# Kernel tuning notes

Measured on AMD Instinct MI355X. Metric: run time of the kernel, lower is better.

Reference implementation:

```python
import jax, jax.numpy as jnp
import numpy as np

B, C, H, W = 4, 4, 1080, 1920


def setup_inputs() -> dict:
    key = jax.random.key(0)
    k1, k2 = jax.random.split(key)
    frame = jax.random.normal(k1, (B, C, H, W), dtype=jnp.float32)
    flow = jax.random.normal(k2, (B, 2, H, W), dtype=jnp.float32)
    return {"frame": frame, "flow": flow}


def _bilinear_warp(frame, flow):
    # TF-addons style dense_image_warp: sample frame at (y - flow_y, x - flow_x),
    # query points clamped to the image rectangle, bilinear interpolation.
    b, c, h, w = frame.shape
    gy = jnp.arange(h, dtype=flow.dtype)
    gx = jnp.arange(w, dtype=flow.dtype)
    qy = jnp.clip(gy[None, :, None] - flow[:, 0], 0.0, h - 1)  # [B,H,W]
    qx = jnp.clip(gx[None, None, :] - flow[:, 1], 0.0, w - 1)  # [B,H,W]
    y0f = jnp.floor(qy)
    x0f = jnp.floor(qx)
    wy = (qy - y0f)[:, None]  # [B,1,H,W]
    wx = (qx - x0f)[:, None]
    y0 = y0f.astype(jnp.int32)
    x0 = x0f.astype(jnp.int32)
    y1 = jnp.minimum(y0 + 1, h - 1)
    x1 = jnp.minimum(x0 + 1, w - 1)
    ff = frame.reshape(b, c, h * w)

    def gather(y, x):
        idx = (y * w + x).reshape(b, 1, h * w)
        return jnp.take_along_axis(ff, idx, axis=2).reshape(b, c, h, w)

    top = gather(y0, x0) * (1.0 - wx) + gather(y0, x1) * wx
    bot = gather(y1, x0) * (1.0 - wx) + gather(y1, x1) * wx
    return top * (1.0 - wy) + bot * wy


def reference(frame, flow):
    return _bilinear_warp(frame, flow)
```

## Files before the change

kernel.cpp:

```cpp
#include <hip/hip_runtime.h>


#define BB 4
#define CC 4
#define HH 1080
#define WW 1920
#define HW (HH * WW)
#define NPIX (BB * HH * WW)
#define NBLK (NPIX / 256)

typedef float f32x2 __attribute__((ext_vector_type(2), aligned(4)));

__global__ __launch_bounds__(256) void dense_warp_kernel(
    const float* __restrict__ frame,
    const float* __restrict__ flow,
    float* __restrict__ out)
{
    const int n   = blockIdx.x;
    const int blk = (n & 7) * (NBLK >> 3) + (n >> 3);

    const int p = blk * 256 + threadIdx.x;
    const int x = p % WW;
    const int t = p / WW;
    const int y = t % HH;
    const int b = t / HH;

    const size_t rowoff = (size_t)y * WW + x;
    const float fy = flow[(size_t)(b * 2 + 0) * HW + rowoff];
    const float fx = flow[(size_t)(b * 2 + 1) * HW + rowoff];

    const float qy = fminf(fmaxf((float)y - fy, 0.0f), (float)(HH - 1));
    const float qx = fminf(fmaxf((float)x - fx, 0.0f), (float)(WW - 1));
    const float y0f = floorf(qy);
    const float x0f = floorf(qx);
    const float wy = qy - y0f;
    float       wx = qx - x0f;
    const int y0 = (int)y0f;
    const int x0 = (int)x0f;
    const int y1 = min(y0 + 1, HH - 1);

    const bool edge = (x0 > WW - 2);
    const int  xb   = edge ? (WW - 2) : x0;
    if (edge) wx = 1.0f;

    const int i0 = y0 * WW + xb;
    const int i1 = y1 * WW + xb;

    const float omwx = 1.0f - wx;
    const float omwy = 1.0f - wy;

#pragma unroll
    for (int c = 0; c < CC; ++c) {
        const float* fp = frame + (size_t)(b * CC + c) * HW;
        const f32x2 t2 = *reinterpret_cast<const f32x2*>(fp + i0);
        const f32x2 b2 = *reinterpret_cast<const f32x2*>(fp + i1);
        const float top = t2.x * omwx + t2.y * wx;
        const float bot = b2.x * omwx + b2.y * wx;
        const float v   = top * omwy + bot * wy;
        __builtin_nontemporal_store(v, out + (size_t)(b * CC + c) * HW + rowoff);
    }
}

extern "C" void kernel_launch(void* const* d_in, const int* in_sizes, int n_in,
                              void* d_out, int out_size, void* d_ws, size_t ws_size,
                              hipStream_t stream)
{
    const float* frame = (const float*)d_in[0];
    const float* flow  = (const float*)d_in[1];
    float* out = (float*)d_out;

    dense_warp_kernel<<<NBLK, 256, 0, stream>>>(frame, flow, out);
}
```

Baseline: 76.65 us.

## Stage frame tiles with halo in LDS for bilinear gathers

Each block now handles a 128x12 output tile and first loads a haloed 23x140 patch of all four channels into shared memory. Bilinear samples whose footprint falls inside the staged patch are read from LDS, and the rest fall back to global memory. The aim is to turn scattered global gathers into cheap LDS reads, since standard-normal flow mostly displaces by only a few pixels. In exchange it adds a staging pass that reads roughly double the tile area, a block-wide barrier, lower occupancy from about 51 KB of LDS per block, and branch divergence on the fallback path.

After: 161.0 us. 110% more time.

```diff
diff --git a/kernel.cpp b/kernel.cpp
--- a/kernel.cpp
+++ b/kernel.cpp
@@ -6,58 +6,118 @@
 #define HH 1080
 #define WW 1920
 #define HW (HH * WW)
-#define NPIX (BB * HH * WW)
-#define NBLK (NPIX / 256)
 
-typedef float f32x2 __attribute__((ext_vector_type(2), aligned(4)));
+#define TW 128
+#define TH 12
+#define MARG 5
+#define RST 23
+#define CST 140
+#define CUSE 139
+#define TILES_X (WW / TW)
+#define TILES_Y (HH / TH)
+#define NBLK (BB * TILES_Y * TILES_X)
+#define STAGE_N (CC * RST * CST)
 
 __global__ __launch_bounds__(256) void dense_warp_kernel(
     const float* __restrict__ frame,
     const float* __restrict__ flow,
     float* __restrict__ out)
 {
+    __shared__ float lds[STAGE_N];
+
     const int n   = blockIdx.x;
     const int blk = (n & 7) * (NBLK >> 3) + (n >> 3);
 
-    const int p = blk * 256 + threadIdx.x;
-    const int x = p % WW;
-    const int t = p / WW;
-    const int y = t % HH;
-    const int b = t / HH;
+    const int txi = blk % TILES_X;
+    const int t2  = blk / TILES_X;
+    const int tyi = t2 % TILES_Y;
+    const int b   = t2 / TILES_Y;
 
-    const size_t rowoff = (size_t)y * WW + x;
-    const float fy = flow[(size_t)(b * 2 + 0) * HW + rowoff];
-    const float fx = flow[(size_t)(b * 2 + 1) * HW + rowoff];
+    const int tx = txi * TW;
+    const int ty = tyi * TH;
+    const int row_base = ty - MARG;
+    const int col_base = tx - MARG;
 
-    const float qy = fminf(fmaxf((float)y - fy, 0.0f), (float)(HH - 1));
-    const float qx = fminf(fmaxf((float)x - fx, 0.0f), (float)(WW - 1));
-    const float y0f = floorf(qy);
-    const float x0f = floorf(qx);
-    const float wy = qy - y0f;
-    float       wx = qx - x0f;
-    const int y0 = (int)y0f;
-    const int x0 = (int)x0f;
-    const int y1 = min(y0 + 1, HH - 1);
+    const float* fb = frame + (size_t)b * CC * HW;
 
-    const bool edge = (x0 > WW - 2);
-    const int  xb   = edge ? (WW - 2) : x0;
-    if (edge) wx = 1.0f;
+    for (int idx = threadIdx.x; idx < STAGE_N; idx += 256) {
+        const int col = idx % CST;
+        const int tt  = idx / CST;
+        const int r   = tt % RST;
+        const int c   = tt / RST;
+        const int grow = min(max(row_base + r, 0), HH - 1);
+        const int gcol = min(max(col_base + col, 0), WW - 1);
+        lds[idx] = fb[(size_t)c * HW + grow * WW + gcol];
+    }
+    __syncthreads();
 
-    const int i0 = y0 * WW + xb;
-    const int i1 = y1 * WW + xb;
-
-    const float omwx = 1.0f - wx;
-    const float omwy = 1.0f - wy;
+    const int x_local = threadIdx.x & (TW - 1);
+    const int rg      = threadIdx.x >> 7;
+    const int x       = tx + x_local;
 
 #pragma unroll
-    for (int c = 0; c < CC; ++c) {
-        const float* fp = frame + (size_t)(b * CC + c) * HW;
-        const f32x2 t2 = *reinterpret_cast<const f32x2*>(fp + i0);
-        const f32x2 b2 = *reinterpret_cast<const f32x2*>(fp + i1);
-        const float top = t2.x * omwx + t2.y * wx;
-        const float bot = b2.x * omwx + b2.y * wx;
-        const float v   = top * omwy + bot * wy;
-        __builtin_nontemporal_store(v, out + (size_t)(b * CC + c) * HW + rowoff);
+    for (int r = 0; r < TH / 2; ++r) {
+        const int y = ty + rg * (TH / 2) + r;
+        const size_t rowoff = (size_t)y * WW + x;
+
+        const float fy = flow[(size_t)(b * 2 + 0) * HW + rowoff];
+        const float fx = flow[(size_t)(b * 2 + 1) * HW + rowoff];
+
+        const float qy  = fminf(fmaxf((float)y - fy, 0.0f), (float)(HH - 1));
+        const float qx  = fminf(fmaxf((float)x - fx, 0.0f), (float)(WW - 1));
+        const float y0f = floorf(qy);
+        const float x0f = floorf(qx);
+        const float wy  = qy - y0f;
+        float       wx  = qx - x0f;
+        const int y0 = (int)y0f;
+        const int x0 = (int)x0f;
+        const int y1 = min(y0 + 1, HH - 1);
+
+        const bool edge = (x0 > WW - 2);
+        const int  xb   = edge ? (WW - 2) : x0;
+        if (edge) wx = 1.0f;
+
+        const float omwx = 1.0f - wx;
+        const float omwy = 1.0f - wy;
+
+        const int sy0 = y0 - row_base;
+        const int sy1 = y1 - row_base;
+        const int sx  = xb - col_base;
+
+        float res[CC];
+        if (sy0 >= 0 && sy1 < RST && sx >= 0 && sx < CUSE - 1) {
+            const int itop = sy0 * CST + sx;
+            const int ibot = sy1 * CST + sx;
+#pragma unroll
+            for (int c = 0; c < CC; ++c) {
+                const float* p  = lds + c * (RST * CST);
+                const float t0 = p[itop];
+                const float t1 = p[itop + 1];
+                const float b0 = p[ibot];
+                const float b1 = p[ibot + 1];
+                res[c] = (t0 * omwx + t1 * wx) * omwy
+                       + (b0 * omwx + b1 * wx) * wy;
+            }
+        } else {
+            const int i0 = y0 * WW + xb;
+            const int i1 = y1 * WW + xb;
+#pragma unroll
+            for (int c = 0; c < CC; ++c) {
+                const float* fp = fb + (size_t)c * HW;
+                const float t0 = fp[i0];
+                const float t1 = fp[i0 + 1];
+                const float b0 = fp[i1];
+                const float b1 = fp[i1 + 1];
+                res[c] = (t0 * omwx + t1 * wx) * omwy
+                       + (b0 * omwx + b1 * wx) * wy;
+            }
+        }
+
+#pragma unroll
+        for (int c = 0; c < CC; ++c) {
+            __builtin_nontemporal_store(
+                res[c], out + (size_t)(b * CC + c) * HW + rowoff);
+        }
     }
 }
 
```

## Add fp16 NHWC prepass so bilinear gather fetches all channels per tap

Applied to the files above, without the earlier changes.

A prepass kernel converts the frame to a channel-interleaved fp16 layout in workspace. The gather kernel then loads two 16-byte vectors, one per row tap, that hold both horizontal neighbours for all four channels, instead of eight scattered fp32 pair loads. This cuts random-access traffic, but it adds a full extra read and write pass over the frame plus a second launch, and it loses precision because values are rounded to fp16. If the workspace is too small, the original fp32 kernel runs as a fallback.

After: 69.91 us. 1.1x faster.

```diff
diff --git a/kernel.cpp b/kernel.cpp
--- a/kernel.cpp
+++ b/kernel.cpp
@@ -6,20 +6,42 @@
 #define HH 1080
 #define WW 1920
 #define HW (HH * WW)
-#define NPIX (BB * HH * WW)
-#define NBLK (NPIX / 256)
+#define NPX (BB * HH * WW)
+#define NBLK (NPX / 256)
+#define WS_BYTES ((size_t)NPX * CC * 2)
 
-typedef float f32x2 __attribute__((ext_vector_type(2), aligned(4)));
+typedef _Float16 h4 __attribute__((ext_vector_type(4), aligned(8)));
+typedef _Float16 h8 __attribute__((ext_vector_type(8), aligned(8)));
 
-__global__ __launch_bounds__(256) void dense_warp_kernel(
+__global__ __launch_bounds__(256) void nhwc_fp16_prepass(
     const float* __restrict__ frame,
+    _Float16* __restrict__ ws)
+{
+    const int n   = blockIdx.x;
+    const int blk = (n & 7) * (NBLK >> 3) + (n >> 3);
+    const int p   = blk * 256 + threadIdx.x;
+    const int x = p % WW;
+    const int t = p / WW;
+    const int y = t % HH;
+    const int b = t / HH;
+
+    const size_t off = (size_t)(b * CC) * HW + (size_t)y * WW + x;
+    h4 o;
+    o[0] = (_Float16)frame[off];
+    o[1] = (_Float16)frame[off + (size_t)HW];
+    o[2] = (_Float16)frame[off + (size_t)(2 * HW)];
+    o[3] = (_Float16)frame[off + (size_t)(3 * HW)];
+    *reinterpret_cast<h4*>(ws + (size_t)p * 4) = o;
+}
+
+__global__ __launch_bounds__(256) void dense_warp_gather(
+    const _Float16* __restrict__ ws,
     const float* __restrict__ flow,
     float* __restrict__ out)
 {
     const int n   = blockIdx.x;
     const int blk = (n & 7) * (NBLK >> 3) + (n >> 3);
-
-    const int p = blk * 256 + threadIdx.x;
+    const int p   = blk * 256 + threadIdx.x;
     const int x = p % WW;
     const int t = p / WW;
     const int y = t % HH;
@@ -29,12 +51,12 @@
     const float fy = flow[(size_t)(b * 2 + 0) * HW + rowoff];
     const float fx = flow[(size_t)(b * 2 + 1) * HW + rowoff];
 
-    const float qy = fminf(fmaxf((float)y - fy, 0.0f), (float)(HH - 1));
-    const float qx = fminf(fmaxf((float)x - fx, 0.0f), (float)(WW - 1));
+    const float qy  = fminf(fmaxf((float)y - fy, 0.0f), (float)(HH - 1));
+    const float qx  = fminf(fmaxf((float)x - fx, 0.0f), (float)(WW - 1));
     const float y0f = floorf(qy);
     const float x0f = floorf(qx);
-    const float wy = qy - y0f;
-    float       wx = qx - x0f;
+    const float wy  = qy - y0f;
+    float       wx  = qx - x0f;
     const int y0 = (int)y0f;
     const int x0 = (int)x0f;
     const int y1 = min(y0 + 1, HH - 1);
@@ -43,9 +65,61 @@
     const int  xb   = edge ? (WW - 2) : x0;
     if (edge) wx = 1.0f;
 
+    const h8 tp = *reinterpret_cast<const h8*>(
+        ws + ((size_t)(b * HH + y0) * WW + xb) * 4);
+    const h8 bt = *reinterpret_cast<const h8*>(
+        ws + ((size_t)(b * HH + y1) * WW + xb) * 4);
+
+    const float omwx = 1.0f - wx;
+    const float omwy = 1.0f - wy;
+
+#pragma unroll
+    for (int c = 0; c < CC; ++c) {
+        const float tl = (float)tp[c];
+        const float tr = (float)tp[c + 4];
+        const float bl = (float)bt[c];
+        const float br = (float)bt[c + 4];
+        const float top = tl * omwx + tr * wx;
+        const float bot = bl * omwx + br * wx;
+        const float v   = top * omwy + bot * wy;
+        __builtin_nontemporal_store(v, out + (size_t)(b * CC + c) * HW + rowoff);
+    }
+}
+
+typedef float f32x2 __attribute__((ext_vector_type(2), aligned(4)));
+
+__global__ __launch_bounds__(256) void dense_warp_fallback(
+    const float* __restrict__ frame,
+    const float* __restrict__ flow,
+    float* __restrict__ out)
+{
+    const int n   = blockIdx.x;
+    const int blk = (n & 7) * (NBLK >> 3) + (n >> 3);
+    const int p   = blk * 256 + threadIdx.x;
+    const int x = p % WW;
+    const int t = p / WW;
+    const int y = t % HH;
+    const int b = t / HH;
+
+    const size_t rowoff = (size_t)y * WW + x;
+    const float fy = flow[(size_t)(b * 2 + 0) * HW + rowoff];
+    const float fx = flow[(size_t)(b * 2 + 1) * HW + rowoff];
+
+    const float qy  = fminf(fmaxf((float)y - fy, 0.0f), (float)(HH - 1));
+    const float qx  = fminf(fmaxf((float)x - fx, 0.0f), (float)(WW - 1));
+    const float y0f = floorf(qy);
+    const float x0f = floorf(qx);
+    const float wy  = qy - y0f;
+    float       wx  = qx - x0f;
+    const int y0 = (int)y0f;
+    const int x0 = (int)x0f;
+    const int y1 = min(y0 + 1, HH - 1);
+    const bool edge = (x0 > WW - 2);
+    const int  xb   = edge ? (WW - 2) : x0;
+    if (edge) wx = 1.0f;
+
     const int i0 = y0 * WW + xb;
     const int i1 = y1 * WW + xb;
-
     const float omwx = 1.0f - wx;
     const float omwy = 1.0f - wy;
 
@@ -69,5 +143,11 @@
     const float* flow  = (const float*)d_in[1];
     float* out = (float*)d_out;
 
-    dense_warp_kernel<<<NBLK, 256, 0, stream>>>(frame, flow, out);
+    if (ws_size >= WS_BYTES && d_ws != nullptr) {
+        _Float16* ws = (_Float16*)d_ws;
+        nhwc_fp16_prepass<<<NBLK, 256, 0, stream>>>(frame, ws);
+        dense_warp_gather<<<NBLK, 256, 0, stream>>>(ws, flow, out);
+    } else {
+        dense_warp_fallback<<<NBLK, 256, 0, stream>>>(frame, flow, out);
+    }
 }
```
